# Performance work log

Hardware: AMD Instinct MI355X
Metric: run time of the kernel (lower is better)

Reference implementation:

```python
import jax, jax.numpy as jnp
import numpy as np

NUM_HEADS = 16
EMBED_DIM = 1024
HEAD_DIM = EMBED_DIM // NUM_HEADS  # 64


def setup_inputs() -> dict:
    key = jax.random.key(0)
    k1, k2, k3 = jax.random.split(key, 3)
    x = jax.random.normal(k1, (2, 2048, EMBED_DIM), dtype=jnp.float32)
    # torch Linear(head_dim, 3*head_dim): weight [3*hd, hd], bias [3*hd]
    # stored here as W_qkv [hd, 3*hd] so that y = x @ W_qkv + b
    lim = 1.0 / np.sqrt(HEAD_DIM)
    W_qkv = jax.random.uniform(k2, (HEAD_DIM, 3 * HEAD_DIM), minval=-lim, maxval=lim, dtype=jnp.float32)
    b_qkv = jax.random.uniform(k3, (3 * HEAD_DIM,), minval=-lim, maxval=lim, dtype=jnp.float32)
    return {"x": x, "W_qkv": W_qkv, "b_qkv": b_qkv}


def reference(x, W_qkv, b_qkv):
    B, T, E = x.shape
    # [B, T, E] -> [B, H, T, hd]
    xh = x.reshape(B, T, NUM_HEADS, HEAD_DIM).transpose(0, 2, 1, 3)
    qkv = xh @ W_qkv + b_qkv  # [B, H, T, 3*hd], shared weights across heads
    q, k, v = jnp.split(qkv, 3, axis=-1)
    scale = 1.0 / jnp.sqrt(jnp.asarray(HEAD_DIM, dtype=x.dtype))
    scores = jnp.einsum('bhqd,bhkd->bhqk', q, k) * scale  # [B, H, T, T]
    attn = jax.nn.softmax(scores, axis=-1)
    out = jnp.einsum('bhqk,bhkd->bhqd', attn, v)  # [B, H, T, hd]
    return out.transpose(0, 2, 1, 3).reshape(B, T, E)
```

## Files before the change

kernel.cpp:

```cpp
#include <hip/hip_runtime.h>
#include <hip/hip_bf16.h>

#define T_SEQ   2048
#define EMBED   1024
#define HD      64
#define NHEADS  16
#define NBH     32
#define QSCALE  0.18033688011112042f

typedef __attribute__((ext_vector_type(8))) short short8;
typedef __attribute__((ext_vector_type(4))) short s16x4;
typedef __attribute__((ext_vector_type(4))) float f32x4;
typedef __attribute__((ext_vector_type(2))) unsigned int uint2v;

#if __has_builtin(__builtin_amdgcn_exp2f)
#define EXP2F __builtin_amdgcn_exp2f
#else
#define EXP2F exp2f
#endif

__device__ __forceinline__ ushort bf16r(float f) {
  union { float f; unsigned u; } v; v.f = f;
  return (ushort)((v.u + 0x8000u) >> 16);
}

__device__ __forceinline__ unsigned pk2bf_perm(float a, float b) {
  union { float f; unsigned u; } ua, ub; ua.f = a; ub.f = b;
  return __builtin_amdgcn_perm(ub.u + 0x8000u, ua.u + 0x8000u, 0x07060302u);
}
#if __has_builtin(__builtin_amdgcn_cvt_pk_bf16_f32)
typedef __attribute__((ext_vector_type(2))) __bf16 bf16x2;
__device__ __forceinline__ unsigned pkbf(float a, float b) {
  union { bf16x2 v; unsigned u; } c;
  c.v = __builtin_amdgcn_cvt_pk_bf16_f32(a, b);
  return c.u;
}
#else
#define pkbf pk2bf_perm
#endif

#if __has_builtin(__builtin_amdgcn_mfma_f32_16x16x16bf16_1k)
__device__ __forceinline__ f32x4 MFMA16(s16x4 A, s16x4 B, f32x4 C) {
  return __builtin_amdgcn_mfma_f32_16x16x16bf16_1k(A, B, C, 0, 0, 0);
}
#else
__device__ __forceinline__ f32x4 MFMA16(s16x4 A, s16x4 B, f32x4 C) {
  short8 a8 = (short8){A[0], A[1], A[2], A[3], 0, 0, 0, 0};
  short8 b8 = (short8){B[0], B[1], B[2], B[3], 0, 0, 0, 0};
  return __builtin_amdgcn_mfma_f32_16x16x32_bf16(a8, b8, C, 0, 0, 0);
}
#endif

__device__ __forceinline__ void async16(const ushort* g, ushort* l) {
  __builtin_amdgcn_global_load_lds(
      (const __attribute__((address_space(1))) unsigned int*)g,
      (__attribute__((address_space(3))) unsigned int*)l, 16, 0, 0);
}

__global__ __launch_bounds__(256) void prep_w(const float* __restrict__ W,
                                              ushort* __restrict__ Wg) {
  const int i = blockIdx.x * 256 + threadIdx.x;
  const int d = i / 192, c = i - d * 192;
  const int phys = c * 64 + (((d >> 3) ^ (c & 7)) << 3) + (d & 7);
  Wg[phys] = bf16r(W[i]);
}

__global__ __launch_bounds__(256) void qkv_proj(
    const float* __restrict__ x, const ushort* __restrict__ Wg,
    const float* __restrict__ bias,
    ushort* __restrict__ Qws, ushort* __restrict__ Kws,
    ushort* __restrict__ Vtws) {
  __shared__ ushort WtL[192 * 64];
  __shared__ float bl[192];

  const int bx = blockIdx.x;
  const int b  = bx >> 9;
  const int h  = (bx >> 5) & 15;
  const int t0 = (bx & 31) * 64;
  const int tid = threadIdx.x;
  const int wave = tid >> 6, lane = tid & 63;
  const int quad = lane >> 4, n16 = lane & 15;

  const int trow = t0 + wave * 16 + n16;
  const float* xr = x + ((size_t)(b * T_SEQ + trow)) * EMBED + h * HD;
  short8 xa[2];
#pragma unroll
  for (int ks = 0; ks < 2; ks++) {
    f32x4 v0 = *(const f32x4*)(xr + ks * 32 + quad * 8);
    f32x4 v1 = *(const f32x4*)(xr + ks * 32 + quad * 8 + 4);
    short8 f;
    ((unsigned*)&f)[0] = pkbf(v0[0], v0[1]);
    ((unsigned*)&f)[1] = pkbf(v0[2], v0[3]);
    ((unsigned*)&f)[2] = pkbf(v1[0], v1[1]);
    ((unsigned*)&f)[3] = pkbf(v1[2], v1[3]);
    xa[ks] = f;
  }

#pragma unroll
  for (int it = 0; it < 6; it++)
    async16(Wg + it * 2048 + tid * 8, WtL + it * 2048 + wave * 512);
  if (tid < 192) bl[tid] = bias[tid];
  __syncthreads();

  const int bh = b * NHEADS + h;
  const size_t qkbase = (size_t)bh * T_SEQ * HD;
  const int tw = t0 + wave * 16;
  const int sw = n16 & 7;

#pragma unroll
  for (int nt = 0; nt < 12; nt++) {
    const ushort* wrow = WtL + (nt * 16 + n16) * 64;
    const short8 wb0 = *(short8*)(wrow + ((quad ^ sw) << 3));
    const short8 wb1 = *(short8*)(wrow + (((4 | quad) ^ sw) << 3));
    const float bv = bl[nt * 16 + n16];
    f32x4 acc = (f32x4){0.f, 0.f, 0.f, 0.f};
    acc = __builtin_amdgcn_mfma_f32_16x16x32_bf16(xa[0], wb0, acc, 0, 0, 0);
    acc = __builtin_amdgcn_mfma_f32_16x16x32_bf16(xa[1], wb1, acc, 0, 0, 0);
    if (nt < 4) {
      const int d = nt * 16 + n16;
#pragma unroll
      for (int r = 0; r < 4; r++)
        Qws[qkbase + (size_t)(tw + quad * 4 + r) * HD + d] =
            bf16r((acc[r] + bv) * QSCALE);
    } else if (nt < 8) {
      const int d = (nt - 4) * 16 + n16;
#pragma unroll
      for (int r = 0; r < 4; r++)
        Kws[qkbase + (size_t)(tw + quad * 4 + r) * HD + d] =
            bf16r(acc[r] + bv);
    } else {
      const int d = (nt - 8) * 16 + n16;
      const int tcol = tw + quad * 4;
      uint2v pk;
      pk.x = pkbf(acc[0] + bv, acc[1] + bv);
      pk.y = pkbf(acc[2] + bv, acc[3] + bv);
      *(uint2v*)(Vtws + (size_t)(bh * HD + d) * T_SEQ + tcol) = pk;
    }
  }
}

__global__ __launch_bounds__(256) void flash_attn(
    const ushort* __restrict__ Qws, const ushort* __restrict__ Kws,
    const ushort* __restrict__ Vtws, float* __restrict__ out) {
  __shared__ ushort Ks[2][64 * 64];
  __shared__ ushort Vs[2][64 * 64];

  const int bx = blockIdx.x;
  const int bh = bx >> 4;
  const int q0 = (bx & 15) * 128;
  const int b = bh >> 4, h = bh & 15;
  const int tid = threadIdx.x;
  const int wave = tid >> 6, lane = tid & 63;
  const int quad = lane >> 4, n16 = lane & 15;

  const ushort* Qb = Qws + (size_t)bh * T_SEQ * HD;
  const ushort* Kb = Kws + (size_t)bh * T_SEQ * HD;
  const ushort* Vb = Vtws + (size_t)bh * HD * T_SEQ;

  short8 qa[2][2];
#pragma unroll
  for (int mt = 0; mt < 2; mt++)
#pragma unroll
    for (int ks = 0; ks < 2; ks++) {
      const int row = q0 + wave * 32 + mt * 16 + n16;
      qa[mt][ks] = *(const short8*)(Qb + (size_t)row * HD + ks * 32 + quad * 8);
    }

  const int sr = tid >> 3, sp = tid & 7;
  const int sl = (sp ^ (sr & 7)) * 8;
  const ushort* srcK0 = Kb + (size_t)sr * HD + sl;
  const ushort* srcK1 = Kb + (size_t)(sr + 32) * HD + sl;
  const ushort* srcV0 = Vb + (size_t)sr * T_SEQ + sl;
  const ushort* srcV1 = Vb + (size_t)(sr + 32) * T_SEQ + sl;

  int koff[2];
#pragma unroll
  for (int ks = 0; ks < 2; ks++)
    koff[ks] = n16 * 64 + ((((ks << 2) | quad) ^ (n16 & 7)) << 3);
  int voff[4];
#pragma unroll
  for (int nt = 0; nt < 4; nt++)
    voff[nt] = n16 * 64 + ((((nt << 1) | (quad >> 1)) ^ (n16 & 7)) << 3) +
               ((quad & 1) << 2);

  f32x4 o[2][4];
  float lsum[2] = {0.f, 0.f};
#pragma unroll
  for (int mt = 0; mt < 2; mt++)
#pragma unroll
    for (int db = 0; db < 4; db++) o[mt][db] = (f32x4){0.f, 0.f, 0.f, 0.f};

  async16(srcK0, Ks[0] + wave * 512);
  async16(srcK1, Ks[0] + 2048 + wave * 512);
  async16(srcV0, Vs[0] + wave * 512);
  async16(srcV1, Vs[0] + 2048 + wave * 512);
  __syncthreads();

  for (int kt = 0; kt < 32; kt++) {
    const int bsel = kt & 1;
    if (kt < 31) {
      const size_t kK = (size_t)(kt + 1) * 64 * HD;
      const size_t kV = (size_t)(kt + 1) * 64;
      async16(srcK0 + kK, Ks[bsel ^ 1] + wave * 512);
      async16(srcK1 + kK, Ks[bsel ^ 1] + 2048 + wave * 512);
      async16(srcV0 + kV, Vs[bsel ^ 1] + wave * 512);
      async16(srcV1 + kV, Vs[bsel ^ 1] + 2048 + wave * 512);
    }
    const ushort* Kt = Ks[bsel];
    const ushort* Vt = Vs[bsel];

    f32x4 s[2][4];
#pragma unroll
    for (int nt = 0; nt < 4; nt++) {
      const short8 ka0 = *(short8*)(Kt + (nt << 10) + koff[0]);
      const short8 ka1 = *(short8*)(Kt + (nt << 10) + koff[1]);
#pragma unroll
      for (int mt = 0; mt < 2; mt++) {
        f32x4 acc = (f32x4){0.f, 0.f, 0.f, 0.f};
        acc = __builtin_amdgcn_mfma_f32_16x16x32_bf16(ka0, qa[mt][0], acc, 0, 0, 0);
        acc = __builtin_amdgcn_mfma_f32_16x16x32_bf16(ka1, qa[mt][1], acc, 0, 0, 0);
        s[mt][nt] = acc;
      }
    }

    s16x4 pb[2][4];
#pragma unroll
    for (int mt = 0; mt < 2; mt++) {
#pragma unroll
      for (int nt = 0; nt < 4; nt++) {
        float p0 = EXP2F(s[mt][nt][0]), p1 = EXP2F(s[mt][nt][1]);
        float p2 = EXP2F(s[mt][nt][2]), p3 = EXP2F(s[mt][nt][3]);
        lsum[mt] += (p0 + p1) + (p2 + p3);
        s16x4 pv;
        ((unsigned*)&pv)[0] = pkbf(p0, p1);
        ((unsigned*)&pv)[1] = pkbf(p2, p3);
        pb[mt][nt] = pv;
      }
    }

#pragma unroll
    for (int db = 0; db < 4; db++) {
      s16x4 va[4];
#pragma unroll
      for (int nt = 0; nt < 4; nt++)
        va[nt] = *(s16x4*)(Vt + (db << 10) + voff[nt]);
#pragma unroll
      for (int mt = 0; mt < 2; mt++)
#pragma unroll
        for (int nt = 0; nt < 4; nt++)
          o[mt][db] = MFMA16(va[nt], pb[mt][nt], o[mt][db]);
    }
    __syncthreads();
  }

#pragma unroll
  for (int mt = 0; mt < 2; mt++) {
    lsum[mt] += __shfl_xor(lsum[mt], 16, 64);
    lsum[mt] += __shfl_xor(lsum[mt], 32, 64);
    const float rl = 1.0f / lsum[mt];
    const int row = q0 + wave * 32 + mt * 16 + n16;
    float* op = out + (size_t)(b * T_SEQ + row) * EMBED + h * HD + quad * 4;
#pragma unroll
    for (int db = 0; db < 4; db++)
      *(f32x4*)(op + db * 16) = o[mt][db] * rl;
  }
}

extern "C" void kernel_launch(void* const* d_in, const int* in_sizes, int n_in,
                              void* d_out, int out_size, void* d_ws, size_t ws_size,
                              hipStream_t stream) {
  (void)in_sizes; (void)n_in; (void)out_size; (void)ws_size;
  const float* x    = (const float*)d_in[0];
  const float* W    = (const float*)d_in[1];
  const float* bias = (const float*)d_in[2];
  float* out = (float*)d_out;

  const size_t elems = (size_t)NBH * T_SEQ * HD;
  ushort* Qws  = (ushort*)d_ws;
  ushort* Kws  = Qws + elems;
  ushort* Vtws = Kws + elems;
  ushort* Wg   = Vtws + elems;

  prep_w<<<dim3(48), dim3(256), 0, stream>>>(W, Wg);
  qkv_proj<<<dim3(1024), dim3(256), 0, stream>>>(x, Wg, bias, Qws, Kws, Vtws);
  flash_attn<<<dim3(512), dim3(256), 0, stream>>>(Qws, Kws, Vtws, out);
}
```

Baseline: 139.9 us.

## Route P through LDS to use 16x16x32 MFMA for PV and halve per-block queries

The flash attention kernel now writes the bf16 probabilities for each wave into a shared-memory tile and reads them back in the A-operand layout. This lets the P·V product use the wider 16x16x32 MFMA in place of the 16x16x16 variant. Each wave now handles 16 query rows instead of 32, so the grid doubles to 1024 blocks, and block indexing interleaves heads so neighbouring blocks work on different heads. The cost is extra LDS traffic and a lower MFMA-to-load ratio per K/V tile, since each loaded tile now serves half as many queries. The output store also changes from vectorized f32x4 writes to scalar writes.

Result: faster. 135.0 us (-3.5%).

```diff
diff --git a/kernel.cpp b/kernel.cpp
--- a/kernel.cpp
+++ b/kernel.cpp
@@ -9,7 +9,6 @@
 #define QSCALE  0.18033688011112042f
 
 typedef __attribute__((ext_vector_type(8))) short short8;
-typedef __attribute__((ext_vector_type(4))) short s16x4;
 typedef __attribute__((ext_vector_type(4))) float f32x4;
 typedef __attribute__((ext_vector_type(2))) unsigned int uint2v;
 
@@ -37,18 +36,6 @@
 }
 #else
 #define pkbf pk2bf_perm
-#endif
-
-#if __has_builtin(__builtin_amdgcn_mfma_f32_16x16x16bf16_1k)
-__device__ __forceinline__ f32x4 MFMA16(s16x4 A, s16x4 B, f32x4 C) {
-  return __builtin_amdgcn_mfma_f32_16x16x16bf16_1k(A, B, C, 0, 0, 0);
-}
-#else
-__device__ __forceinline__ f32x4 MFMA16(s16x4 A, s16x4 B, f32x4 C) {
-  short8 a8 = (short8){A[0], A[1], A[2], A[3], 0, 0, 0, 0};
-  short8 b8 = (short8){B[0], B[1], B[2], B[3], 0, 0, 0, 0};
-  return __builtin_amdgcn_mfma_f32_16x16x32_bf16(a8, b8, C, 0, 0, 0);
-}
 #endif
 
 __device__ __forceinline__ void async16(const ushort* g, ushort* l) {
@@ -144,10 +131,11 @@
     const ushort* __restrict__ Vtws, float* __restrict__ out) {
   __shared__ ushort Ks[2][64 * 64];
   __shared__ ushort Vs[2][64 * 64];
+  __shared__ ushort Ps[4 * 16 * 64];
 
   const int bx = blockIdx.x;
-  const int bh = bx >> 4;
-  const int q0 = (bx & 15) * 128;
+  const int bh = bx & 31;
+  const int q0 = (bx >> 5) * 64;
   const int b = bh >> 4, h = bh & 15;
   const int tid = threadIdx.x;
   const int wave = tid >> 6, lane = tid & 63;
@@ -157,14 +145,12 @@
   const ushort* Kb = Kws + (size_t)bh * T_SEQ * HD;
   const ushort* Vb = Vtws + (size_t)bh * HD * T_SEQ;
 
-  short8 qa[2][2];
-#pragma unroll
-  for (int mt = 0; mt < 2; mt++)
-#pragma unroll
-    for (int ks = 0; ks < 2; ks++) {
-      const int row = q0 + wave * 32 + mt * 16 + n16;
-      qa[mt][ks] = *(const short8*)(Qb + (size_t)row * HD + ks * 32 + quad * 8);
-    }
+  short8 qa[2];
+#pragma unroll
+  for (int ks = 0; ks < 2; ks++) {
+    const int row = q0 + wave * 16 + n16;
+    qa[ks] = *(const short8*)(Qb + (size_t)row * HD + ks * 32 + quad * 8);
+  }
 
   const int sr = tid >> 3, sp = tid & 7;
   const int sl = (sp ^ (sr & 7)) * 8;
@@ -173,22 +159,17 @@
   const ushort* srcV0 = Vb + (size_t)sr * T_SEQ + sl;
   const ushort* srcV1 = Vb + (size_t)(sr + 32) * T_SEQ + sl;
 
-  int koff[2];
+  int foff[2];
 #pragma unroll
   for (int ks = 0; ks < 2; ks++)
-    koff[ks] = n16 * 64 + ((((ks << 2) | quad) ^ (n16 & 7)) << 3);
-  int voff[4];
-#pragma unroll
-  for (int nt = 0; nt < 4; nt++)
-    voff[nt] = n16 * 64 + ((((nt << 1) | (quad >> 1)) ^ (n16 & 7)) << 3) +
-               ((quad & 1) << 2);
-
-  f32x4 o[2][4];
-  float lsum[2] = {0.f, 0.f};
-#pragma unroll
-  for (int mt = 0; mt < 2; mt++)
-#pragma unroll
-    for (int db = 0; db < 4; db++) o[mt][db] = (f32x4){0.f, 0.f, 0.f, 0.f};
+    foff[ks] = n16 * 64 + ((((ks << 2) | quad) ^ (n16 & 7)) << 3);
+
+  f32x4 o[4];
+  float lsum = 0.f;
+#pragma unroll
+  for (int nt = 0; nt < 4; nt++) o[nt] = (f32x4){0.f, 0.f, 0.f, 0.f};
+
+  ushort* Pw = Ps + wave * 1024;
 
   async16(srcK0, Ks[0] + wave * 512);
   async16(srcK1, Ks[0] + 2048 + wave * 512);
@@ -209,60 +190,56 @@
     const ushort* Kt = Ks[bsel];
     const ushort* Vt = Vs[bsel];
 
-    f32x4 s[2][4];
-#pragma unroll
-    for (int nt = 0; nt < 4; nt++) {
-      const short8 ka0 = *(short8*)(Kt + (nt << 10) + koff[0]);
-      const short8 ka1 = *(short8*)(Kt + (nt << 10) + koff[1]);
-#pragma unroll
-      for (int mt = 0; mt < 2; mt++) {
-        f32x4 acc = (f32x4){0.f, 0.f, 0.f, 0.f};
-        acc = __builtin_amdgcn_mfma_f32_16x16x32_bf16(ka0, qa[mt][0], acc, 0, 0, 0);
-        acc = __builtin_amdgcn_mfma_f32_16x16x32_bf16(ka1, qa[mt][1], acc, 0, 0, 0);
-        s[mt][nt] = acc;
-      }
-    }
-
-    s16x4 pb[2][4];
-#pragma unroll
-    for (int mt = 0; mt < 2; mt++) {
-#pragma unroll
-      for (int nt = 0; nt < 4; nt++) {
-        float p0 = EXP2F(s[mt][nt][0]), p1 = EXP2F(s[mt][nt][1]);
-        float p2 = EXP2F(s[mt][nt][2]), p3 = EXP2F(s[mt][nt][3]);
-        lsum[mt] += (p0 + p1) + (p2 + p3);
-        s16x4 pv;
-        ((unsigned*)&pv)[0] = pkbf(p0, p1);
-        ((unsigned*)&pv)[1] = pkbf(p2, p3);
-        pb[mt][nt] = pv;
-      }
-    }
-
-#pragma unroll
-    for (int db = 0; db < 4; db++) {
-      s16x4 va[4];
-#pragma unroll
-      for (int nt = 0; nt < 4; nt++)
-        va[nt] = *(s16x4*)(Vt + (db << 10) + voff[nt]);
-#pragma unroll
-      for (int mt = 0; mt < 2; mt++)
-#pragma unroll
-        for (int nt = 0; nt < 4; nt++)
-          o[mt][db] = MFMA16(va[nt], pb[mt][nt], o[mt][db]);
+    f32x4 s[4];
+#pragma unroll
+    for (int nt = 0; nt < 4; nt++) {
+      const short8 ka0 = *(short8*)(Kt + (nt << 10) + foff[0]);
+      const short8 ka1 = *(short8*)(Kt + (nt << 10) + foff[1]);
+      f32x4 acc = (f32x4){0.f, 0.f, 0.f, 0.f};
+      acc = __builtin_amdgcn_mfma_f32_16x16x32_bf16(ka0, qa[0], acc, 0, 0, 0);
+      acc = __builtin_amdgcn_mfma_f32_16x16x32_bf16(ka1, qa[1], acc, 0, 0, 0);
+      s[nt] = acc;
+    }
+
+#pragma unroll
+    for (int nt = 0; nt < 4; nt++) {
+      float p0 = EXP2F(s[nt][0]), p1 = EXP2F(s[nt][1]);
+      float p2 = EXP2F(s[nt][2]), p3 = EXP2F(s[nt][3]);
+      lsum += (p0 + p1) + (p2 + p3);
+      uint2v pk;
+      pk.x = pkbf(p0, p1);
+      pk.y = pkbf(p2, p3);
+      *(uint2v*)(Pw + n16 * 64 +
+                 ((((nt << 1) | (quad >> 1)) ^ (n16 & 7)) << 3) +
+                 ((quad & 1) << 2)) = pk;
+    }
+
+    short8 pa0 = *(short8*)(Pw + foff[0]);
+    short8 pa1 = *(short8*)(Pw + foff[1]);
+#pragma unroll
+    for (int nt = 0; nt < 4; nt++) {
+      const short8 vb0 = *(short8*)(Vt + (nt << 10) + foff[0]);
+      const short8 vb1 = *(short8*)(Vt + (nt << 10) + foff[1]);
+      o[nt] = __builtin_amdgcn_mfma_f32_16x16x32_bf16(pa0, vb0, o[nt], 0, 0, 0);
+      o[nt] = __builtin_amdgcn_mfma_f32_16x16x32_bf16(pa1, vb1, o[nt], 0, 0, 0);
     }
     __syncthreads();
   }
 
-#pragma unroll
-  for (int mt = 0; mt < 2; mt++) {
-    lsum[mt] += __shfl_xor(lsum[mt], 16, 64);
-    lsum[mt] += __shfl_xor(lsum[mt], 32, 64);
-    const float rl = 1.0f / lsum[mt];
-    const int row = q0 + wave * 32 + mt * 16 + n16;
-    float* op = out + (size_t)(b * T_SEQ + row) * EMBED + h * HD + quad * 4;
-#pragma unroll
-    for (int db = 0; db < 4; db++)
-      *(f32x4*)(op + db * 16) = o[mt][db] * rl;
+  lsum += __shfl_xor(lsum, 16, 64);
+  lsum += __shfl_xor(lsum, 32, 64);
+  float* Lw = (float*)Pw;
+  if (lane < 16) Lw[n16] = lsum;
+
+#pragma unroll
+  for (int r = 0; r < 4; r++) {
+    const int row = q0 + wave * 16 + quad * 4 + r;
+    const float rl = 1.0f / Lw[quad * 4 + r];
+#pragma unroll
+    for (int nt = 0; nt < 4; nt++) {
+      const int d = nt * 16 + n16;
+      out[(size_t)(b * T_SEQ + row) * EMBED + h * HD + d] = o[nt][r] * rl;
+    }
   }
 }
 
@@ -283,5 +260,5 @@
 
   prep_w<<<dim3(48), dim3(256), 0, stream>>>(W, Wg);
   qkv_proj<<<dim3(1024), dim3(256), 0, stream>>>(x, Wg, bias, Qws, Kws, Vtws);
-  flash_attn<<<dim3(512), dim3(256), 0, stream>>>(Qws, Kws, Vtws, out);
-}
+  flash_attn<<<dim3(1024), dim3(256), 0, stream>>>(Qws, Kws, Vtws, out);
+}
```

## Split attention key range across waves and route P through LDS for wide MFMA

Applied to the files above, without the earlier changes.

Each block now handles 64 query rows with four waves: two split the queries and two split every key tile, and the partial outputs and row sums are merged through LDS at the end. The grid doubles to 1024 blocks with a per-CU occupancy hint. V is no longer staged in shared memory but read straight from global into registers. P goes through a per-wave LDS tile so the PV product can use the 16x16x32 MFMA instead of 16x16x16. The final stores become scalar and strided, and the added LDS round trip for P adds latency.

Measured after the change: 148.4 us. 1.06x slower.

```diff
diff --git a/kernel.cpp b/kernel.cpp
--- a/kernel.cpp
+++ b/kernel.cpp
@@ -9,7 +9,6 @@
 #define QSCALE  0.18033688011112042f
 
 typedef __attribute__((ext_vector_type(8))) short short8;
-typedef __attribute__((ext_vector_type(4))) short s16x4;
 typedef __attribute__((ext_vector_type(4))) float f32x4;
 typedef __attribute__((ext_vector_type(2))) unsigned int uint2v;
 
@@ -37,18 +36,6 @@
 }
 #else
 #define pkbf pk2bf_perm
-#endif
-
-#if __has_builtin(__builtin_amdgcn_mfma_f32_16x16x16bf16_1k)
-__device__ __forceinline__ f32x4 MFMA16(s16x4 A, s16x4 B, f32x4 C) {
-  return __builtin_amdgcn_mfma_f32_16x16x16bf16_1k(A, B, C, 0, 0, 0);
-}
-#else
-__device__ __forceinline__ f32x4 MFMA16(s16x4 A, s16x4 B, f32x4 C) {
-  short8 a8 = (short8){A[0], A[1], A[2], A[3], 0, 0, 0, 0};
-  short8 b8 = (short8){B[0], B[1], B[2], B[3], 0, 0, 0, 0};
-  return __builtin_amdgcn_mfma_f32_16x16x32_bf16(a8, b8, C, 0, 0, 0);
-}
 #endif
 
 __device__ __forceinline__ void async16(const ushort* g, ushort* l) {
@@ -139,19 +126,20 @@
   }
 }
 
-__global__ __launch_bounds__(256) void flash_attn(
+__global__ __launch_bounds__(256, 4) void flash_attn(
     const ushort* __restrict__ Qws, const ushort* __restrict__ Kws,
     const ushort* __restrict__ Vtws, float* __restrict__ out) {
   __shared__ ushort Ks[2][64 * 64];
-  __shared__ ushort Vs[2][64 * 64];
+  __shared__ ushort Ps[4][32 * 40];
 
   const int bx = blockIdx.x;
-  const int bh = bx >> 4;
-  const int q0 = (bx & 15) * 128;
+  const int bh = bx & 31;
+  const int q0 = (bx >> 5) * 64;
   const int b = bh >> 4, h = bh & 15;
   const int tid = threadIdx.x;
   const int wave = tid >> 6, lane = tid & 63;
   const int quad = lane >> 4, n16 = lane & 15;
+  const int qh = wave & 1, kh = wave >> 1;
 
   const ushort* Qb = Qws + (size_t)bh * T_SEQ * HD;
   const ushort* Kb = Kws + (size_t)bh * T_SEQ * HD;
@@ -162,7 +150,7 @@
   for (int mt = 0; mt < 2; mt++)
 #pragma unroll
     for (int ks = 0; ks < 2; ks++) {
-      const int row = q0 + wave * 32 + mt * 16 + n16;
+      const int row = q0 + qh * 32 + mt * 16 + n16;
       qa[mt][ks] = *(const short8*)(Qb + (size_t)row * HD + ks * 32 + quad * 8);
     }
 
@@ -170,99 +158,127 @@
   const int sl = (sp ^ (sr & 7)) * 8;
   const ushort* srcK0 = Kb + (size_t)sr * HD + sl;
   const ushort* srcK1 = Kb + (size_t)(sr + 32) * HD + sl;
-  const ushort* srcV0 = Vb + (size_t)sr * T_SEQ + sl;
-  const ushort* srcV1 = Vb + (size_t)(sr + 32) * T_SEQ + sl;
-
-  int koff[2];
-#pragma unroll
-  for (int ks = 0; ks < 2; ks++)
-    koff[ks] = n16 * 64 + ((((ks << 2) | quad) ^ (n16 & 7)) << 3);
-  int voff[4];
+
+  int koff[2][2];
+#pragma unroll
+  for (int kt = 0; kt < 2; kt++)
+#pragma unroll
+    for (int ks = 0; ks < 2; ks++)
+      koff[kt][ks] = (kh * 32 + kt * 16 + n16) * 64 +
+                     ((((ks << 2) | quad) ^ (n16 & 7)) << 3);
+
+  const ushort* vp[4];
 #pragma unroll
   for (int nt = 0; nt < 4; nt++)
-    voff[nt] = n16 * 64 + ((((nt << 1) | (quad >> 1)) ^ (n16 & 7)) << 3) +
-               ((quad & 1) << 2);
+    vp[nt] = Vb + (size_t)(nt * 16 + n16) * T_SEQ + kh * 32 + quad * 8;
 
   f32x4 o[2][4];
   float lsum[2] = {0.f, 0.f};
 #pragma unroll
   for (int mt = 0; mt < 2; mt++)
 #pragma unroll
-    for (int db = 0; db < 4; db++) o[mt][db] = (f32x4){0.f, 0.f, 0.f, 0.f};
+    for (int nt = 0; nt < 4; nt++) o[mt][nt] = (f32x4){0.f, 0.f, 0.f, 0.f};
+
+  ushort* Pw = Ps[wave];
 
   async16(srcK0, Ks[0] + wave * 512);
   async16(srcK1, Ks[0] + 2048 + wave * 512);
-  async16(srcV0, Vs[0] + wave * 512);
-  async16(srcV1, Vs[0] + 2048 + wave * 512);
   __syncthreads();
 
   for (int kt = 0; kt < 32; kt++) {
     const int bsel = kt & 1;
     if (kt < 31) {
       const size_t kK = (size_t)(kt + 1) * 64 * HD;
-      const size_t kV = (size_t)(kt + 1) * 64;
       async16(srcK0 + kK, Ks[bsel ^ 1] + wave * 512);
       async16(srcK1 + kK, Ks[bsel ^ 1] + 2048 + wave * 512);
-      async16(srcV0 + kV, Vs[bsel ^ 1] + wave * 512);
-      async16(srcV1 + kV, Vs[bsel ^ 1] + 2048 + wave * 512);
     }
     const ushort* Kt = Ks[bsel];
-    const ushort* Vt = Vs[bsel];
-
-    f32x4 s[2][4];
-#pragma unroll
-    for (int nt = 0; nt < 4; nt++) {
-      const short8 ka0 = *(short8*)(Kt + (nt << 10) + koff[0]);
-      const short8 ka1 = *(short8*)(Kt + (nt << 10) + koff[1]);
+
+    short8 vb[4];
+#pragma unroll
+    for (int nt = 0; nt < 4; nt++) { vb[nt] = *(const short8*)vp[nt]; vp[nt] += 64; }
+
+    f32x4 s[2][2];
+#pragma unroll
+    for (int k2 = 0; k2 < 2; k2++) {
+      const short8 ka0 = *(short8*)(Kt + koff[k2][0]);
+      const short8 ka1 = *(short8*)(Kt + koff[k2][1]);
 #pragma unroll
       for (int mt = 0; mt < 2; mt++) {
         f32x4 acc = (f32x4){0.f, 0.f, 0.f, 0.f};
         acc = __builtin_amdgcn_mfma_f32_16x16x32_bf16(ka0, qa[mt][0], acc, 0, 0, 0);
         acc = __builtin_amdgcn_mfma_f32_16x16x32_bf16(ka1, qa[mt][1], acc, 0, 0, 0);
-        s[mt][nt] = acc;
+        s[mt][k2] = acc;
       }
     }
 
-    s16x4 pb[2][4];
+#pragma unroll
+    for (int mt = 0; mt < 2; mt++)
+#pragma unroll
+      for (int k2 = 0; k2 < 2; k2++) {
+        float p0 = EXP2F(s[mt][k2][0]), p1 = EXP2F(s[mt][k2][1]);
+        float p2 = EXP2F(s[mt][k2][2]), p3 = EXP2F(s[mt][k2][3]);
+        lsum[mt] += (p0 + p1) + (p2 + p3);
+        uint2v pk;
+        pk.x = pkbf(p0, p1);
+        pk.y = pkbf(p2, p3);
+        *(uint2v*)(Pw + (mt * 16 + n16) * 40 + k2 * 16 + quad * 4) = pk;
+      }
+
+    short8 pa[2];
+#pragma unroll
+    for (int mt = 0; mt < 2; mt++)
+      pa[mt] = *(short8*)(Pw + (mt * 16 + n16) * 40 + quad * 8);
+#pragma unroll
+    for (int nt = 0; nt < 4; nt++)
+#pragma unroll
+      for (int mt = 0; mt < 2; mt++)
+        o[mt][nt] = __builtin_amdgcn_mfma_f32_16x16x32_bf16(pa[mt], vb[nt],
+                                                            o[mt][nt], 0, 0, 0);
+    __syncthreads();
+  }
+
+  if (wave >= 2) {
+    float* Oex = ((float*)Ks) + (wave - 2) * 2048;
+#pragma unroll
+    for (int mt = 0; mt < 2; mt++)
+#pragma unroll
+      for (int nt = 0; nt < 4; nt++)
+        *(f32x4*)(Oex + ((mt * 4 + nt) << 8) + (lane << 2)) = o[mt][nt];
+    float* lx = (float*)Pw;
+    lx[lane * 2] = lsum[0]; lx[lane * 2 + 1] = lsum[1];
+  }
+  __syncthreads();
+  if (wave < 2) {
+    float* Oex = ((float*)Ks) + wave * 2048;
+    const float* lx = (const float*)Ps[wave + 2];
+    lsum[0] += lx[lane * 2]; lsum[1] += lx[lane * 2 + 1];
+#pragma unroll
+    for (int mt = 0; mt < 2; mt++)
+#pragma unroll
+      for (int nt = 0; nt < 4; nt++)
+        o[mt][nt] += *(f32x4*)(Oex + ((mt * 4 + nt) << 8) + (lane << 2));
+
 #pragma unroll
     for (int mt = 0; mt < 2; mt++) {
-#pragma unroll
-      for (int nt = 0; nt < 4; nt++) {
-        float p0 = EXP2F(s[mt][nt][0]), p1 = EXP2F(s[mt][nt][1]);
-        float p2 = EXP2F(s[mt][nt][2]), p3 = EXP2F(s[mt][nt][3]);
-        lsum[mt] += (p0 + p1) + (p2 + p3);
-        s16x4 pv;
-        ((unsigned*)&pv)[0] = pkbf(p0, p1);
-        ((unsigned*)&pv)[1] = pkbf(p2, p3);
-        pb[mt][nt] = pv;
+      lsum[mt] += __shfl_xor(lsum[mt], 16, 64);
+      lsum[mt] += __shfl_xor(lsum[mt], 32, 64);
+    }
+    float* Lw = (float*)Pw;
+    if (lane < 16) { Lw[n16] = lsum[0]; Lw[16 + n16] = lsum[1]; }
+
+#pragma unroll
+    for (int mt = 0; mt < 2; mt++)
+#pragma unroll
+      for (int r = 0; r < 4; r++) {
+        const int row = q0 + qh * 32 + mt * 16 + quad * 4 + r;
+        const float rl = 1.0f / Lw[mt * 16 + quad * 4 + r];
+#pragma unroll
+        for (int nt = 0; nt < 4; nt++) {
+          const int d = nt * 16 + n16;
+          out[(size_t)(b * T_SEQ + row) * EMBED + h * HD + d] = o[mt][nt][r] * rl;
+        }
       }
-    }
-
-#pragma unroll
-    for (int db = 0; db < 4; db++) {
-      s16x4 va[4];
-#pragma unroll
-      for (int nt = 0; nt < 4; nt++)
-        va[nt] = *(s16x4*)(Vt + (db << 10) + voff[nt]);
-#pragma unroll
-      for (int mt = 0; mt < 2; mt++)
-#pragma unroll
-        for (int nt = 0; nt < 4; nt++)
-          o[mt][db] = MFMA16(va[nt], pb[mt][nt], o[mt][db]);
-    }
-    __syncthreads();
-  }
-
-#pragma unroll
-  for (int mt = 0; mt < 2; mt++) {
-    lsum[mt] += __shfl_xor(lsum[mt], 16, 64);
-    lsum[mt] += __shfl_xor(lsum[mt], 32, 64);
-    const float rl = 1.0f / lsum[mt];
-    const int row = q0 + wave * 32 + mt * 16 + n16;
-    float* op = out + (size_t)(b * T_SEQ + row) * EMBED + h * HD + quad * 4;
-#pragma unroll
-    for (int db = 0; db < 4; db++)
-      *(f32x4*)(op + db * 16) = o[mt][db] * rl;
   }
 }
 
@@ -283,5 +299,5 @@
 
   prep_w<<<dim3(48), dim3(256), 0, stream>>>(W, Wg);
   qkv_proj<<<dim3(1024), dim3(256), 0, stream>>>(x, Wg, bias, Qws, Kws, Vtws);
-  flash_attn<<<dim3(512), dim3(256), 0, stream>>>(Qws, Kws, Vtws, out);
-}
+  flash_attn<<<dim3(1024), dim3(256), 0, stream>>>(Qws, Kws, Vtws, out);
+}
```
